# Performance work log

Measured on AMD Instinct MI355X. Metric: run time of the kernel, lower is better.

Reference implementation:

```python
import jax, jax.numpy as jnp
import numpy as np

# 8-neighbor shift offsets (dy, dx) encoded by the 11x11 one-hot kernels with padding=5
OFFSETS = [(-5, 0), (-1, 0), (0, 5), (0, 1), (5, 0), (1, 0), (0, -5), (0, -1)]
PROP_TIME = 24
PAD = 5


def _shift(p, dy, dx, H, W):
    # p is zero-padded by PAD on the last two dims; out(y,x) = in(y+dy, x+dx)
    return p[..., PAD + dy:PAD + dy + H, PAD + dx:PAD + dx + W]


def _grep(depth):
    # depth: (B,1,H,W) -> (B,8,H,W): gather the 8 shifted copies (grep_conv)
    B, _, H, W = depth.shape
    p = jnp.pad(depth[:, 0], ((0, 0), (PAD, PAD), (PAD, PAD)))
    return jnp.stack([_shift(p, dy, dx, H, W) for dy, dx in OFFSETS], axis=1)


def _spn(g):
    # g: (B,8,H,W) -> (B,8,H,W): channel-wise shift (diagonal spn kernel, spn_conv)
    B, C, H, W = g.shape
    p = jnp.pad(g, ((0, 0), (0, 0), (PAD, PAD), (PAD, PAD)))
    return jnp.stack([_shift(p[:, c], dy, dx, H, W)
                      for c, (dy, dx) in enumerate(OFFSETS)], axis=1)


def setup_inputs() -> dict:
    key = jax.random.key(0)
    k1, k2, k3, k4 = jax.random.split(key, 4)
    B, H, W = 8, 768, 768
    guidance = jax.random.normal(k1, (B, 8, H, W), dtype=jnp.float32)
    blur_depth = jax.random.uniform(k2, (B, 1, H, W), dtype=jnp.float32)
    vals = jax.random.uniform(k3, (B, 1, H, W), dtype=jnp.float32) * 10.0
    mask = jax.random.uniform(k4, (B, 1, H, W)) < 0.05
    sparse_depth = jnp.where(mask, vals, 0.0)
    return {"guidance": guidance, "blur_depth": blur_depth, "sparse_depth": sparse_depth}


def reference(guidance, blur_depth, sparse_depth):
    # affinity_normalization (norm_type='8sum': no abs on guidance)
    gate_wb = _spn(guidance)                                      # (B,8,H,W)
    abs_weight = jnp.sum(jnp.abs(gate_wb), axis=1, keepdims=True)  # (B,1,H,W)
    gate_wb = gate_wb / jnp.clip(abs_weight, 1e-6)
    gate_sum = jnp.sum(gate_wb, axis=1, keepdims=True)             # (B,1,H,W)

    sparse_mask = jnp.sign(sparse_depth)
    raw = blur_depth
    result = blur_depth
    for _ in range(PROP_TIME):
        neigh = _grep(result)                                      # (B,8,H,W)
        result = jnp.sum(gate_wb * neigh, axis=1, keepdims=True)   # weighted sum
        result = (1.0 - gate_sum) * raw + result                   # '8sum' residual
        result = (1.0 - sparse_mask) * result + sparse_mask * raw  # sparse blend
    return result
```

## Files before the change

### kernel.cpp

```cpp
#include <hip/hip_runtime.h>


#define HH 768
#define WW 768
#define BATCH 8
#define PLANE (HH * WW)
#define TOTAL (BATCH * PLANE)
#define NG (TOTAL / 4)
#define NITER 24

#define DYS {-5, -1, 0, 0, 5, 1, 0, 0}
#define DXS {0, 0, 5, 1, 0, 0, -5, -1}

typedef _Float16 half8 __attribute__((ext_vector_type(8)));
typedef float f4 __attribute__((ext_vector_type(4)));

__device__ __forceinline__ f4 ldf4(const float* p) { return *(const f4*)p; }

__global__ __launch_bounds__(192) void precompute_kernel(
    const float* __restrict__ g,
    const float* __restrict__ blur,
    const float* __restrict__ sparse,
    half8* __restrict__ wout,
    float* __restrict__ bias)
{
    const int x0 = 4 * threadIdx.x;
    const int y  = blockIdx.y;
    const int b  = blockIdx.z;
    const float* gb = g + (size_t)b * 8 * PLANE;
    const int rowb = y * WW;
    const int pidx = b * PLANE + rowb + x0;
    const int pg   = pidx >> 2;

    f4 wv[8];
    if (x0 >= 8 && x0 <= 756) {
        const f4 zero = (f4)0.f;
        wv[0] = (y >= 5)      ? ldf4(gb + 0 * PLANE + (y - 5) * WW + x0) : zero;
        wv[1] = (y >= 1)      ? ldf4(gb + 1 * PLANE + (y - 1) * WW + x0) : zero;
        wv[4] = (y <= HH - 6) ? ldf4(gb + 4 * PLANE + (y + 5) * WW + x0) : zero;
        wv[5] = (y <= HH - 2) ? ldf4(gb + 5 * PLANE + (y + 1) * WW + x0) : zero;
        {
            f4 a = ldf4(gb + 2 * PLANE + rowb + x0 + 4);
            f4 bq = ldf4(gb + 2 * PLANE + rowb + x0 + 8);
            wv[2] = f4{a[1], a[2], a[3], bq[0]};
        }
        {
            f4 a = ldf4(gb + 3 * PLANE + rowb + x0);
            f4 bq = ldf4(gb + 3 * PLANE + rowb + x0 + 4);
            wv[3] = f4{a[1], a[2], a[3], bq[0]};
        }
        {
            f4 a = ldf4(gb + 6 * PLANE + rowb + x0 - 8);
            f4 bq = ldf4(gb + 6 * PLANE + rowb + x0 - 4);
            wv[6] = f4{a[3], bq[0], bq[1], bq[2]};
        }
        {
            f4 a = ldf4(gb + 7 * PLANE + rowb + x0 - 4);
            f4 bq = ldf4(gb + 7 * PLANE + rowb + x0);
            wv[7] = f4{a[3], bq[0], bq[1], bq[2]};
        }
    } else {
        const int dy[8] = DYS;
        const int dx[8] = DXS;
#pragma unroll
        for (int c = 0; c < 8; ++c) {
#pragma unroll
            for (int j = 0; j < 4; ++j) {
                int yy = y + dy[c];
                int xx = x0 + j + dx[c];
                float v = 0.f;
                if (yy >= 0 && yy < HH && xx >= 0 && xx < WW)
                    v = gb[c * PLANE + yy * WW + xx];
                wv[c][j] = v;
            }
        }
    }

    f4 raw = ldf4(blur + pidx);
    f4 sd  = ldf4(sparse + pidx);
    f4 bout;
#pragma unroll
    for (int j = 0; j < 4; ++j) {
        float abssum = 0.f;
#pragma unroll
        for (int c = 0; c < 8; ++c) abssum += fabsf(wv[c][j]);
        float inv = 1.f / fmaxf(abssum, 1e-6f);
        float gs = 0.f;
#pragma unroll
        for (int c = 0; c < 8; ++c) gs += wv[c][j] * inv;
        float s = sd[j];
        float m = (s > 0.f) ? 1.f : ((s < 0.f) ? -1.f : 0.f);
        float A = 1.f - m;
        bout[j] = (A * (1.f - gs) + m) * raw[j];
        float Ai = A * inv;
        half8 hv;
#pragma unroll
        for (int c = 0; c < 8; ++c) hv[c] = (_Float16)(Ai * wv[c][j]);
        wout[(size_t)j * NG + pg] = hv;
    }
    *(f4*)(bias + pidx) = bout;
}

__global__ __launch_bounds__(192) void step_kernel(
    const half8* __restrict__ w,
    const float* __restrict__ bias,
    const float* __restrict__ prev,
    float* __restrict__ next)
{
    const int L  = blockIdx.x;
    const int b  = L & 7;
    const int y  = L >> 3;
    const int x0 = 4 * threadIdx.x;
    const int rowb = y * WW;
    const int pidx = b * PLANE + rowb + x0;
    const int pg   = pidx >> 2;
    const float* pb = prev + b * PLANE;

    half8 hv0 = w[0 * (size_t)NG + pg];
    half8 hv1 = w[1 * (size_t)NG + pg];
    half8 hv2 = w[2 * (size_t)NG + pg];
    half8 hv3 = w[3 * (size_t)NG + pg];
    f4 acc = ldf4(bias + pidx);

    if (x0 >= 8 && x0 <= 756) {
        const f4 zero = (f4)0.f;
        f4 um5 = (y >= 5)      ? ldf4(pb + (y - 5) * WW + x0) : zero;
        f4 um1 = (y >= 1)      ? ldf4(pb + (y - 1) * WW + x0) : zero;
        f4 dp5 = (y <= HH - 6) ? ldf4(pb + (y + 5) * WW + x0) : zero;
        f4 dp1 = (y <= HH - 2) ? ldf4(pb + (y + 1) * WW + x0) : zero;
        f4 m2 = ldf4(pb + rowb + x0 - 8);
        f4 m1 = ldf4(pb + rowb + x0 - 4);
        f4 c0 = ldf4(pb + rowb + x0);
        f4 p1 = ldf4(pb + rowb + x0 + 4);
        f4 p2 = ldf4(pb + rowb + x0 + 8);
        f4 tm5 = f4{m2[3], m1[0], m1[1], m1[2]};
        f4 tm1 = f4{m1[3], c0[0], c0[1], c0[2]};
        f4 tp1 = f4{c0[1], c0[2], c0[3], p1[0]};
        f4 tp5 = f4{p1[1], p1[2], p1[3], p2[0]};

        acc[0] = fmaf((float)hv0[0], um5[0], acc[0]);
        acc[1] = fmaf((float)hv1[0], um5[1], acc[1]);
        acc[2] = fmaf((float)hv2[0], um5[2], acc[2]);
        acc[3] = fmaf((float)hv3[0], um5[3], acc[3]);

        acc[0] = fmaf((float)hv0[1], um1[0], acc[0]);
        acc[1] = fmaf((float)hv1[1], um1[1], acc[1]);
        acc[2] = fmaf((float)hv2[1], um1[2], acc[2]);
        acc[3] = fmaf((float)hv3[1], um1[3], acc[3]);

        acc[0] = fmaf((float)hv0[2], tp5[0], acc[0]);
        acc[1] = fmaf((float)hv1[2], tp5[1], acc[1]);
        acc[2] = fmaf((float)hv2[2], tp5[2], acc[2]);
        acc[3] = fmaf((float)hv3[2], tp5[3], acc[3]);

        acc[0] = fmaf((float)hv0[3], tp1[0], acc[0]);
        acc[1] = fmaf((float)hv1[3], tp1[1], acc[1]);
        acc[2] = fmaf((float)hv2[3], tp1[2], acc[2]);
        acc[3] = fmaf((float)hv3[3], tp1[3], acc[3]);

        acc[0] = fmaf((float)hv0[4], dp5[0], acc[0]);
        acc[1] = fmaf((float)hv1[4], dp5[1], acc[1]);
        acc[2] = fmaf((float)hv2[4], dp5[2], acc[2]);
        acc[3] = fmaf((float)hv3[4], dp5[3], acc[3]);

        acc[0] = fmaf((float)hv0[5], dp1[0], acc[0]);
        acc[1] = fmaf((float)hv1[5], dp1[1], acc[1]);
        acc[2] = fmaf((float)hv2[5], dp1[2], acc[2]);
        acc[3] = fmaf((float)hv3[5], dp1[3], acc[3]);

        acc[0] = fmaf((float)hv0[6], tm5[0], acc[0]);
        acc[1] = fmaf((float)hv1[6], tm5[1], acc[1]);
        acc[2] = fmaf((float)hv2[6], tm5[2], acc[2]);
        acc[3] = fmaf((float)hv3[6], tm5[3], acc[3]);

        acc[0] = fmaf((float)hv0[7], tm1[0], acc[0]);
        acc[1] = fmaf((float)hv1[7], tm1[1], acc[1]);
        acc[2] = fmaf((float)hv2[7], tm1[2], acc[2]);
        acc[3] = fmaf((float)hv3[7], tm1[3], acc[3]);
    } else {
        const int dy[8] = DYS;
        const int dx[8] = DXS;
        half8 hvs[4] = {hv0, hv1, hv2, hv3};
#pragma unroll
        for (int j = 0; j < 4; ++j) {
#pragma unroll
            for (int c = 0; c < 8; ++c) {
                int yy = y + dy[c];
                int xx = x0 + j + dx[c];
                float n = 0.f;
                if (yy >= 0 && yy < HH && xx >= 0 && xx < WW)
                    n = pb[yy * WW + xx];
                acc[j] = fmaf((float)hvs[j][c], n, acc[j]);
            }
        }
    }
    *(f4*)(next + pidx) = acc;
}

__global__ __launch_bounds__(256) void step_recompute_kernel(
    const float* __restrict__ g,
    const float* __restrict__ blur,
    const float* __restrict__ sparse,
    const float* __restrict__ prev,
    float* __restrict__ next)
{
    const int dy[8] = DYS;
    const int dx[8] = DXS;
    int x = blockIdx.x * blockDim.x + threadIdx.x;
    int y = blockIdx.y;
    int b = blockIdx.z;
    if (x >= WW) return;

    const float* gb = g + (size_t)b * 8 * PLANE;
    float w[8];
    float abssum = 0.f;
#pragma unroll
    for (int c = 0; c < 8; ++c) {
        int yy = y + dy[c];
        int xx = x + dx[c];
        float v = 0.f;
        if (yy >= 0 && yy < HH && xx >= 0 && xx < WW)
            v = gb[c * PLANE + yy * WW + xx];
        w[c] = v;
        abssum += fabsf(v);
    }
    float inv = 1.f / fmaxf(abssum, 1e-6f);
    float gs = 0.f;
#pragma unroll
    for (int c = 0; c < 8; ++c) {
        w[c] *= inv;
        gs += w[c];
    }
    int pidx = b * PLANE + y * WW + x;
    float sd = sparse[pidx];
    float m = (sd > 0.f) ? 1.f : ((sd < 0.f) ? -1.f : 0.f);
    float A = 1.f - m;
    float raw = blur[pidx];

    const float* pb = prev + b * PLANE;
    float acc = 0.f;
#pragma unroll
    for (int c = 0; c < 8; ++c) {
        int yy = y + dy[c];
        int xx = x + dx[c];
        float n = 0.f;
        if (yy >= 0 && yy < HH && xx >= 0 && xx < WW)
            n = pb[yy * WW + xx];
        acc = fmaf(A * w[c], n, acc);
    }
    next[pidx] = acc + (A * (1.f - gs) + m) * raw;
}

extern "C" void kernel_launch(void* const* d_in, const int* in_sizes, int n_in,
                              void* d_out, int out_size, void* d_ws, size_t ws_size,
                              hipStream_t stream) {
    const float* g      = (const float*)d_in[0];
    const float* blur   = (const float*)d_in[1];
    const float* sparse = (const float*)d_in[2];
    float* out = (float*)d_out;

    dim3 blockPre(192, 1, 1);
    dim3 gridPre(1, HH, BATCH);

    dim3 blockStep(192, 1, 1);
    dim3 gridStep(HH * BATCH, 1, 1);

    const size_t need_fast = (size_t)TOTAL * 16 + (size_t)TOTAL * 4 * 2;

    if (ws_size >= need_fast) {
        half8* w    = (half8*)d_ws;
        float* bias = (float*)((char*)d_ws + (size_t)TOTAL * 16);
        float* r0   = bias + TOTAL;

        precompute_kernel<<<gridPre, blockPre, 0, stream>>>(g, blur, sparse, w, bias);

        const float* prev = blur;
        for (int it = 0; it < NITER; ++it) {
            float* nxt = (it % 2 == 0) ? r0 : out;
            step_kernel<<<gridStep, blockStep, 0, stream>>>(w, bias, prev, nxt);
            prev = nxt;
        }
    } else {
        dim3 block2(256, 1, 1);
        dim3 grid2(WW / 256, HH, BATCH);
        float* r0 = (float*)d_ws;
        const float* prev = blur;
        for (int it = 0; it < NITER; ++it) {
            float* nxt = (it % 2 == 0) ? r0 : out;
            step_recompute_kernel<<<grid2, block2, 0, stream>>>(g, blur, sparse,
                                                                prev, nxt);
            prev = nxt;
        }
    }
}
```

Baseline: 748.5 us.

## Fuse precompute and all iterations into one persistent cooperative kernel

Replaces the 25 separate launches with one cooperative persistent kernel that precomputes the fp16 weights, then runs all 24 propagation steps, separated by grid-wide syncs. Each block owns a fixed band of rows. It keeps the bias in registers and part of its weights in LDS, and only the remainder of the weights is reread from global memory on each step. This removes launch gaps and cuts weight and bias traffic, at the cost of 24 grid barriers and the risk of falling back if occupancy is below 4 blocks per CU.

```diff
diff --git a/kernel.cpp b/kernel.cpp
--- a/kernel.cpp
+++ b/kernel.cpp
@@ -1,4 +1,7 @@
 #include <hip/hip_runtime.h>
+#include <hip/hip_cooperative_groups.h>
+
+namespace cg = cooperative_groups;
 
 
 #define HH 768
@@ -9,6 +12,16 @@
 #define NG (TOTAL / 4)
 #define NITER 24
 
+#define PBLOCKS 1024
+#define PTHREADS 256
+#define RPB 6
+#define GPR 192
+#define GPB (RPB * GPR)
+#define NCHUNK 5
+#define LDSC 2
+#define GLOB_GPB (GPB - LDSC * PTHREADS)
+#define NGW ((size_t)PBLOCKS * GLOB_GPB)
+
 #define DYS {-5, -1, 0, 0, 5, 1, 0, 0}
 #define DXS {0, 0, 5, 1, 0, 0, -5, -1}
 
@@ -16,6 +29,238 @@
 typedef float f4 __attribute__((ext_vector_type(4)));
 
 __device__ __forceinline__ f4 ldf4(const float* p) { return *(const f4*)p; }
+__device__ __forceinline__ f4 sel4(int c, f4 v) { return c ? v : (f4)0.f; }
+
+__global__ __launch_bounds__(PTHREADS, 4) void persist_kernel(
+    const float* __restrict__ g,
+    const float* __restrict__ blur,
+    const float* __restrict__ sparse,
+    half8* __restrict__ wg,
+    float* __restrict__ r0,
+    float* __restrict__ r1,
+    float* __restrict__ out)
+{
+    __shared__ half8 lds_w[4][LDSC * PTHREADS];
+
+    cg::grid_group grid = cg::this_grid();
+
+    const int L       = blockIdx.x;
+    const int batch   = L & 7;
+    const int band    = L >> 3;
+    const int rowbase = band * RPB;
+    const int tid     = threadIdx.x;
+    const float* gb   = g + (size_t)batch * 8 * PLANE;
+
+    f4 bias_r[NCHUNK];
+
+#pragma unroll
+    for (int k = 0; k < NCHUNK; ++k) {
+        bias_r[k] = (f4)0.f;
+        const int gl = k * PTHREADS + tid;
+        if (gl < GPB) {
+            const int yo   = gl / GPR;
+            const int xg   = gl - yo * GPR;
+            const int y    = rowbase + yo;
+            const int x0   = 4 * xg;
+            const int rowb = y * WW;
+            const int pidx = batch * PLANE + rowb + x0;
+
+            f4 wv[8];
+            if (x0 >= 8 && x0 <= 756) {
+                const int ya = (y >= 5)      ? y - 5 : y;
+                const int yb = (y >= 1)      ? y - 1 : y;
+                const int yc = (y <= HH - 6) ? y + 5 : y;
+                const int yd = (y <= HH - 2) ? y + 1 : y;
+                wv[0] = sel4(y >= 5,      ldf4(gb + 0 * PLANE + ya * WW + x0));
+                wv[1] = sel4(y >= 1,      ldf4(gb + 1 * PLANE + yb * WW + x0));
+                wv[4] = sel4(y <= HH - 6, ldf4(gb + 4 * PLANE + yc * WW + x0));
+                wv[5] = sel4(y <= HH - 2, ldf4(gb + 5 * PLANE + yd * WW + x0));
+                {
+                    f4 a  = ldf4(gb + 2 * PLANE + rowb + x0 + 4);
+                    f4 bq = ldf4(gb + 2 * PLANE + rowb + x0 + 8);
+                    wv[2] = f4{a[1], a[2], a[3], bq[0]};
+                }
+                {
+                    f4 a  = ldf4(gb + 3 * PLANE + rowb + x0);
+                    f4 bq = ldf4(gb + 3 * PLANE + rowb + x0 + 4);
+                    wv[3] = f4{a[1], a[2], a[3], bq[0]};
+                }
+                {
+                    f4 a  = ldf4(gb + 6 * PLANE + rowb + x0 - 8);
+                    f4 bq = ldf4(gb + 6 * PLANE + rowb + x0 - 4);
+                    wv[6] = f4{a[3], bq[0], bq[1], bq[2]};
+                }
+                {
+                    f4 a  = ldf4(gb + 7 * PLANE + rowb + x0 - 4);
+                    f4 bq = ldf4(gb + 7 * PLANE + rowb + x0);
+                    wv[7] = f4{a[3], bq[0], bq[1], bq[2]};
+                }
+            } else {
+                const int dy[8] = DYS;
+                const int dx[8] = DXS;
+#pragma unroll
+                for (int c = 0; c < 8; ++c) {
+#pragma unroll
+                    for (int j = 0; j < 4; ++j) {
+                        int yy = y + dy[c];
+                        int xx = x0 + j + dx[c];
+                        float v = 0.f;
+                        if (yy >= 0 && yy < HH && xx >= 0 && xx < WW)
+                            v = gb[c * PLANE + yy * WW + xx];
+                        wv[c][j] = v;
+                    }
+                }
+            }
+
+            f4 raw = ldf4(blur + pidx);
+            f4 sd  = ldf4(sparse + pidx);
+            f4 bout;
+#pragma unroll
+            for (int j = 0; j < 4; ++j) {
+                float abssum = 0.f;
+#pragma unroll
+                for (int c = 0; c < 8; ++c) abssum += fabsf(wv[c][j]);
+                float inv = 1.f / fmaxf(abssum, 1e-6f);
+                float gs = 0.f;
+#pragma unroll
+                for (int c = 0; c < 8; ++c) gs += wv[c][j] * inv;
+                float s = sd[j];
+                float m = (s > 0.f) ? 1.f : ((s < 0.f) ? -1.f : 0.f);
+                float A = 1.f - m;
+                bout[j] = (A * (1.f - gs) + m) * raw[j];
+                float Ai = A * inv;
+                half8 hv;
+#pragma unroll
+                for (int c = 0; c < 8; ++c) hv[c] = (_Float16)(Ai * wv[c][j]);
+                if (k < LDSC)
+                    lds_w[j][k * PTHREADS + tid] = hv;
+                else
+                    wg[(size_t)j * NGW + (size_t)L * GLOB_GPB +
+                       (gl - LDSC * PTHREADS)] = hv;
+            }
+            bias_r[k] = bout;
+        }
+    }
+
+    __threadfence();
+    grid.sync();
+
+    const float* prev = blur;
+    for (int it = 0; it < NITER; ++it) {
+        float* nxt = (it == NITER - 1) ? out : ((it & 1) ? r1 : r0);
+        const float* pb = prev + (size_t)batch * PLANE;
+
+#pragma unroll
+        for (int k = 0; k < NCHUNK; ++k) {
+            const int gl = k * PTHREADS + tid;
+            if (gl < GPB) {
+                const int yo   = gl / GPR;
+                const int xg   = gl - yo * GPR;
+                const int y    = rowbase + yo;
+                const int x0   = 4 * xg;
+                const int rowb = y * WW;
+                const int pidx = batch * PLANE + rowb + x0;
+
+                half8 hv0, hv1, hv2, hv3;
+                if (k < LDSC) {
+                    hv0 = lds_w[0][k * PTHREADS + tid];
+                    hv1 = lds_w[1][k * PTHREADS + tid];
+                    hv2 = lds_w[2][k * PTHREADS + tid];
+                    hv3 = lds_w[3][k * PTHREADS + tid];
+                } else {
+                    const size_t wb = (size_t)L * GLOB_GPB +
+                                      (gl - LDSC * PTHREADS);
+                    hv0 = wg[0 * NGW + wb];
+                    hv1 = wg[1 * NGW + wb];
+                    hv2 = wg[2 * NGW + wb];
+                    hv3 = wg[3 * NGW + wb];
+                }
+                f4 acc = bias_r[k];
+
+                if (x0 >= 8 && x0 <= 756) {
+                    const int ya = (y >= 5)      ? y - 5 : y;
+                    const int yb = (y >= 1)      ? y - 1 : y;
+                    const int yc = (y <= HH - 6) ? y + 5 : y;
+                    const int yd = (y <= HH - 2) ? y + 1 : y;
+                    f4 um5 = sel4(y >= 5,      ldf4(pb + ya * WW + x0));
+                    f4 um1 = sel4(y >= 1,      ldf4(pb + yb * WW + x0));
+                    f4 dp5 = sel4(y <= HH - 6, ldf4(pb + yc * WW + x0));
+                    f4 dp1 = sel4(y <= HH - 2, ldf4(pb + yd * WW + x0));
+                    f4 m2 = ldf4(pb + rowb + x0 - 8);
+                    f4 m1 = ldf4(pb + rowb + x0 - 4);
+                    f4 c0 = ldf4(pb + rowb + x0);
+                    f4 p1 = ldf4(pb + rowb + x0 + 4);
+                    f4 p2 = ldf4(pb + rowb + x0 + 8);
+                    f4 tm5 = f4{m2[3], m1[0], m1[1], m1[2]};
+                    f4 tm1 = f4{m1[3], c0[0], c0[1], c0[2]};
+                    f4 tp1 = f4{c0[1], c0[2], c0[3], p1[0]};
+                    f4 tp5 = f4{p1[1], p1[2], p1[3], p2[0]};
+
+                    acc[0] = fmaf((float)hv0[0], um5[0], acc[0]);
+                    acc[1] = fmaf((float)hv1[0], um5[1], acc[1]);
+                    acc[2] = fmaf((float)hv2[0], um5[2], acc[2]);
+                    acc[3] = fmaf((float)hv3[0], um5[3], acc[3]);
+
+                    acc[0] = fmaf((float)hv0[1], um1[0], acc[0]);
+                    acc[1] = fmaf((float)hv1[1], um1[1], acc[1]);
+                    acc[2] = fmaf((float)hv2[1], um1[2], acc[2]);
+                    acc[3] = fmaf((float)hv3[1], um1[3], acc[3]);
+
+                    acc[0] = fmaf((float)hv0[2], tp5[0], acc[0]);
+                    acc[1] = fmaf((float)hv1[2], tp5[1], acc[1]);
+                    acc[2] = fmaf((float)hv2[2], tp5[2], acc[2]);
+                    acc[3] = fmaf((float)hv3[2], tp5[3], acc[3]);
+
+                    acc[0] = fmaf((float)hv0[3], tp1[0], acc[0]);
+                    acc[1] = fmaf((float)hv1[3], tp1[1], acc[1]);
+                    acc[2] = fmaf((float)hv2[3], tp1[2], acc[2]);
+                    acc[3] = fmaf((float)hv3[3], tp1[3], acc[3]);
+
+                    acc[0] = fmaf((float)hv0[4], dp5[0], acc[0]);
+                    acc[1] = fmaf((float)hv1[4], dp5[1], acc[1]);
+                    acc[2] = fmaf((float)hv2[4], dp5[2], acc[2]);
+                    acc[3] = fmaf((float)hv3[4], dp5[3], acc[3]);
+
+                    acc[0] = fmaf((float)hv0[5], dp1[0], acc[0]);
+                    acc[1] = fmaf((float)hv1[5], dp1[1], acc[1]);
+                    acc[2] = fmaf((float)hv2[5], dp1[2], acc[2]);
+                    acc[3] = fmaf((float)hv3[5], dp1[3], acc[3]);
+
+                    acc[0] = fmaf((float)hv0[6], tm5[0], acc[0]);
+                    acc[1] = fmaf((float)hv1[6], tm5[1], acc[1]);
+                    acc[2] = fmaf((float)hv2[6], tm5[2], acc[2]);
+                    acc[3] = fmaf((float)hv3[6], tm5[3], acc[3]);
+
+                    acc[0] = fmaf((float)hv0[7], tm1[0], acc[0]);
+                    acc[1] = fmaf((float)hv1[7], tm1[1], acc[1]);
+                    acc[2] = fmaf((float)hv2[7], tm1[2], acc[2]);
+                    acc[3] = fmaf((float)hv3[7], tm1[3], acc[3]);
+                } else {
+                    const int dy[8] = DYS;
+                    const int dx[8] = DXS;
+                    half8 hvs[4] = {hv0, hv1, hv2, hv3};
+#pragma unroll
+                    for (int j = 0; j < 4; ++j) {
+#pragma unroll
+                        for (int c = 0; c < 8; ++c) {
+                            int yy = y + dy[c];
+                            int xx = x0 + j + dx[c];
+                            float n = 0.f;
+                            if (yy >= 0 && yy < HH && xx >= 0 && xx < WW)
+                                n = pb[yy * WW + xx];
+                            acc[j] = fmaf((float)hvs[j][c], n, acc[j]);
+                        }
+                    }
+                }
+                *(f4*)(nxt + pidx) = acc;
+            }
+        }
+
+        __threadfence();
+        grid.sync();
+        prev = nxt;
+    }
+}
 
 __global__ __launch_bounds__(192) void precompute_kernel(
     const float* __restrict__ g,
@@ -39,26 +284,18 @@
         wv[1] = (y >= 1)      ? ldf4(gb + 1 * PLANE + (y - 1) * WW + x0) : zero;
         wv[4] = (y <= HH - 6) ? ldf4(gb + 4 * PLANE + (y + 5) * WW + x0) : zero;
         wv[5] = (y <= HH - 2) ? ldf4(gb + 5 * PLANE + (y + 1) * WW + x0) : zero;
-        {
-            f4 a = ldf4(gb + 2 * PLANE + rowb + x0 + 4);
+        {   f4 a = ldf4(gb + 2 * PLANE + rowb + x0 + 4);
             f4 bq = ldf4(gb + 2 * PLANE + rowb + x0 + 8);
-            wv[2] = f4{a[1], a[2], a[3], bq[0]};
-        }
-        {
-            f4 a = ldf4(gb + 3 * PLANE + rowb + x0);
+            wv[2] = f4{a[1], a[2], a[3], bq[0]}; }
+        {   f4 a = ldf4(gb + 3 * PLANE + rowb + x0);
             f4 bq = ldf4(gb + 3 * PLANE + rowb + x0 + 4);
-            wv[3] = f4{a[1], a[2], a[3], bq[0]};
-        }
-        {
-            f4 a = ldf4(gb + 6 * PLANE + rowb + x0 - 8);
+            wv[3] = f4{a[1], a[2], a[3], bq[0]}; }
+        {   f4 a = ldf4(gb + 6 * PLANE + rowb + x0 - 8);
             f4 bq = ldf4(gb + 6 * PLANE + rowb + x0 - 4);
-            wv[6] = f4{a[3], bq[0], bq[1], bq[2]};
-        }
-        {
-            f4 a = ldf4(gb + 7 * PLANE + rowb + x0 - 4);
+            wv[6] = f4{a[3], bq[0], bq[1], bq[2]}; }
+        {   f4 a = ldf4(gb + 7 * PLANE + rowb + x0 - 4);
             f4 bq = ldf4(gb + 7 * PLANE + rowb + x0);
-            wv[7] = f4{a[3], bq[0], bq[1], bq[2]};
-        }
+            wv[7] = f4{a[3], bq[0], bq[1], bq[2]}; }
     } else {
         const int dy[8] = DYS;
         const int dx[8] = DXS;
@@ -142,37 +379,30 @@
         acc[1] = fmaf((float)hv1[0], um5[1], acc[1]);
         acc[2] = fmaf((float)hv2[0], um5[2], acc[2]);
         acc[3] = fmaf((float)hv3[0], um5[3], acc[3]);
-
         acc[0] = fmaf((float)hv0[1], um1[0], acc[0]);
         acc[1] = fmaf((float)hv1[1], um1[1], acc[1]);
         acc[2] = fmaf((float)hv2[1], um1[2], acc[2]);
         acc[3] = fmaf((float)hv3[1], um1[3], acc[3]);
-
         acc[0] = fmaf((float)hv0[2], tp5[0], acc[0]);
         acc[1] = fmaf((float)hv1[2], tp5[1], acc[1]);
         acc[2] = fmaf((float)hv2[2], tp5[2], acc[2]);
         acc[3] = fmaf((float)hv3[2], tp5[3], acc[3]);
-
         acc[0] = fmaf((float)hv0[3], tp1[0], acc[0]);
         acc[1] = fmaf((float)hv1[3], tp1[1], acc[1]);
         acc[2] = fmaf((float)hv2[3], tp1[2], acc[2]);
         acc[3] = fmaf((float)hv3[3], tp1[3], acc[3]);
-
         acc[0] = fmaf((float)hv0[4], dp5[0], acc[0]);
         acc[1] = fmaf((float)hv1[4], dp5[1], acc[1]);
         acc[2] = fmaf((float)hv2[4], dp5[2], acc[2]);
         acc[3] = fmaf((float)hv3[4], dp5[3], acc[3]);
-
         acc[0] = fmaf((float)hv0[5], dp1[0], acc[0]);
         acc[1] = fmaf((float)hv1[5], dp1[1], acc[1]);
         acc[2] = fmaf((float)hv2[5], dp1[2], acc[2]);
         acc[3] = fmaf((float)hv3[5], dp1[3], acc[3]);
-
         acc[0] = fmaf((float)hv0[6], tm5[0], acc[0]);
         acc[1] = fmaf((float)hv1[6], tm5[1], acc[1]);
         acc[2] = fmaf((float)hv2[6], tm5[2], acc[2]);
         acc[3] = fmaf((float)hv3[6], tm5[3], acc[3]);
-
         acc[0] = fmaf((float)hv0[7], tm1[0], acc[0]);
         acc[1] = fmaf((float)hv1[7], tm1[1], acc[1]);
         acc[2] = fmaf((float)hv2[7], tm1[2], acc[2]);
@@ -259,15 +489,38 @@
     const float* sparse = (const float*)d_in[2];
     float* out = (float*)d_out;
 
-    dim3 blockPre(192, 1, 1);
-    dim3 gridPre(1, HH, BATCH);
-
-    dim3 blockStep(192, 1, 1);
-    dim3 gridStep(HH * BATCH, 1, 1);
-
     const size_t need_fast = (size_t)TOTAL * 16 + (size_t)TOTAL * 4 * 2;
 
     if (ws_size >= need_fast) {
+        int maxB = 0;
+        hipError_t oe = hipOccupancyMaxActiveBlocksPerMultiprocessor(
+            &maxB, persist_kernel, PTHREADS, 0);
+        if (oe == hipSuccess && maxB >= 4) {
+            const size_t wgBytes = (size_t)4 * NGW * sizeof(half8);
+            half8* wg = (half8*)d_ws;
+            float* r0 = (float*)((char*)d_ws + wgBytes);
+            float* r1 = r0 + TOTAL;
+
+            void* args[7];
+            args[0] = (void*)&g;
+            args[1] = (void*)&blur;
+            args[2] = (void*)&sparse;
+            args[3] = (void*)&wg;
+            args[4] = (void*)&r0;
+            args[5] = (void*)&r1;
+            args[6] = (void*)&out;
+
+            hipError_t le = hipLaunchCooperativeKernel(
+                (const void*)persist_kernel, dim3(PBLOCKS), dim3(PTHREADS),
+                args, 0, stream);
+            if (le == hipSuccess) return;
+        }
+
+        dim3 blockPre(192, 1, 1);
+        dim3 gridPre(1, HH, BATCH);
+        dim3 blockStep(192, 1, 1);
+        dim3 gridStep(HH * BATCH, 1, 1);
+
         half8* w    = (half8*)d_ws;
         float* bias = (float*)((char*)d_ws + (size_t)TOTAL * 16);
         float* r0   = bias + TOTAL;
```

Result: no change. 748.8 us (+0.0%).
